# Kernel optimization log

Measured on AMD Instinct MI355X. Metric: run time of the kernel, lower is better.

The kernel has to match this reference:

```python
import jax, jax.numpy as jnp
import numpy as np

H, W = 512, 512
K = 10
N_ACTIONS = 8
HID1, HID2, HIDP = 32, 64, 32
# 8-neighborhood directions (i_dot, j_dot), as in env.DIRS
DIRS = [(-1, -1), (-1, 0), (-1, 1), (0, -1), (0, 1), (1, -1), (1, 0), (1, 1)]


def setup_inputs() -> dict:
    key = jax.random.key(0)
    ks = jax.random.split(key, 16)
    n_state = H * W
    w = lambda k, shape: (jax.random.normal(k, shape, dtype=jnp.float32) * 0.02)
    return {
        "x": jax.random.uniform(ks[0], (3, H, W), dtype=jnp.float32),
        "pos": jax.random.randint(ks[1], (2,), 0, H, dtype=jnp.int32),
        "W1": w(ks[2], (HID1, 3 * n_state)), "b1": jnp.zeros((HID1,), jnp.float32),
        "W2": w(ks[3], (HID2, HID1)), "b2": jnp.zeros((HID2,), jnp.float32),
        "Wro": w(ks[4], (n_state, HID2)), "bro": jnp.zeros((n_state,), jnp.float32),
        "Wri": w(ks[5], (n_state, HID2)), "bri": jnp.zeros((n_state,), jnp.float32),
        "Wp": w(ks[6], (n_state, HID2)), "bp": jnp.zeros((n_state,), jnp.float32),
        "Wpol": w(ks[7], (HIDP, 4 * n_state)), "bpol": jnp.zeros((HIDP,), jnp.float32),
        "Whead": w(ks[8], (N_ACTIONS, HIDP)), "bhead": jnp.zeros((N_ACTIONS,), jnp.float32),
    }


def reference(x, pos, W1, b1, W2, b2, Wro, bro, Wri, bri, Wp, bp, Wpol, bpol, Whead, bhead):
    state = x.reshape(-1)  # (3*H*W,)
    h = jax.nn.relu(W1 @ state + b1)
    h = jax.nn.relu(W2 @ h + b2)
    r_out = jax.nn.sigmoid(Wro @ h + bro).reshape(H, W)
    r_in = jax.nn.sigmoid(Wri @ h + bri).reshape(H, W)
    p = jax.nn.sigmoid(Wp @ h + bp).reshape(H, W)

    p_pad = jnp.pad(p, 1)
    rin_pad = jnp.pad(r_in, 1)
    rout_pad = jnp.pad(r_out, 1)

    def step(v, _):
        v_pad = jnp.pad(v, 1)  # (H+2, W+2)
        cands = []
        for i_dot, j_dot in DIRS:
            xs = j_dot + 1  # note: original code uses j_dot along axis 0
            ys = i_dot + 1
            cands.append(
                v_pad[xs:xs + H, ys:ys + W] * p_pad[xs:xs + H, ys:ys + W]
                + rin_pad[xs:xs + H, ys:ys + W] - rout_pad[xs:xs + H, ys:ys + W]
            )
        return jnp.max(jnp.stack(cands, 0), axis=0), None

    v, _ = jax.lax.scan(step, jnp.zeros((H, W), jnp.float32), None, length=K)

    inp_pol = jnp.concatenate([v.reshape(-1), state])  # (4*H*W,)
    logits = Whead @ jax.nn.relu(Wpol @ inp_pol + bpol) + bhead
    action_prob = jax.nn.softmax(logits, axis=-1)
    state_value = v[pos[0], pos[1]]
    return action_prob, state_value
```

## Files before the change

kernel.cpp:

```cpp
#include <hip/hip_runtime.h>

#define HW 512
#define NSTATE (HW * HW)
#define NC4_X 196608
#define NC4_POLROW 262144
#define NC4_V 65536

#define CH4 1024
#define NCH_X 192
#define SPAN_ROP 1024

#define WS_PART1 0
#define WS_PARTP 6144
#define WS_H2 14336
#define WS_P 14400
#define WS_RD (WS_P + NSTATE)
#define WS_V (WS_RD + NSTATE)

#define SGB __builtin_amdgcn_sched_group_barrier

__device__ __forceinline__ float wred(float a) {
  a += __shfl_xor(a, 32);
  a += __shfl_xor(a, 16);
  a += __shfl_xor(a, 8);
  a += __shfl_xor(a, 4);
  a += __shfl_xor(a, 2);
  a += __shfl_xor(a, 1);
  return a;
}

__device__ __forceinline__ float span_dot(const float4* __restrict__ wp,
                                          const float4* __restrict__ xp) {
  float acc = 0.f;
#pragma unroll
  for (int bt = 0; bt < 2; ++bt) {
    float4 w[8], xv[8];
#pragma unroll
    for (int j = 0; j < 8; ++j) w[j] = wp[bt * 512 + j * 64];
#pragma unroll
    for (int j = 0; j < 8; ++j) xv[j] = xp[bt * 512 + j * 64];
    SGB(0x020, 16, 0);
#pragma unroll
    for (int j = 0; j < 8; ++j)
      acc += w[j].x * xv[j].x + w[j].y * xv[j].y + w[j].z * xv[j].z +
             w[j].w * xv[j].w;
  }
  return acc;
}

__global__ __launch_bounds__(256) void mv_w1(const float4* __restrict__ W1,
                                             const float4* __restrict__ x,
                                             float* __restrict__ part1) {
  int b = blockIdx.x;
  int row = b / 48, cb = b - row * 48;
  int tid = threadIdx.x, wave = tid >> 6, lane = tid & 63;
  int ch = cb * 4 + wave;
  const float4* __restrict__ wp =
      W1 + (size_t)row * NC4_X + (size_t)ch * CH4 + lane;
  const float4* __restrict__ xp = x + (size_t)ch * CH4 + lane;
  float acc = span_dot(wp, xp);
  acc = wred(acc);
  if (lane == 0) part1[ch * 32 + row] = acc;
}

__global__ __launch_bounds__(1024) void finish_h(
    const float* __restrict__ partials, const float* __restrict__ b1,
    const float* __restrict__ W2, const float* __restrict__ b2,
    float* __restrict__ h2out) {
  __shared__ float red[32][32];
  __shared__ float h1[32];
  int tid = threadIdx.x;
  int row = tid & 31, grp = tid >> 5;
  float s = 0.f;
  for (int b = grp; b < NCH_X; b += 32) s += partials[b * 32 + row];
  red[grp][row] = s;
  __syncthreads();
  if (tid < 32) {
    float t = b1[tid];
    for (int g = 0; g < 32; ++g) t += red[g][tid];
    h1[tid] = fmaxf(t, 0.f);
  }
  __syncthreads();
  if (tid < 64) {
    float t = b2[tid];
    for (int k = 0; k < 32; ++k) t += W2[tid * 32 + k] * h1[k];
    h2out[tid] = fmaxf(t, 0.f);
  }
}

__global__ __launch_bounds__(256) void rop_kernel(
    const float4* __restrict__ Wro4, const float* __restrict__ bro,
    const float4* __restrict__ Wri4, const float* __restrict__ bri,
    const float4* __restrict__ Wp4, const float* __restrict__ bp,
    const float* __restrict__ h2, float* __restrict__ p_out,
    float* __restrict__ rd_out) {
  __shared__ float dots[4][3][64];
  int tid = threadIdx.x;
  int wave = tid >> 6, lane = tid & 63;
  int grp = lane >> 4;
  float4 h4 = ((const float4*)h2)[lane & 15];
  int span = blockIdx.x * 4 + wave;
  size_t base = (size_t)span * SPAN_ROP;
  const float4* mats[3] = {Wro4, Wri4, Wp4};
#pragma unroll
  for (int m = 0; m < 3; ++m) {
    const float4* __restrict__ W = mats[m] + base + lane;
#pragma unroll
    for (int batch = 0; batch < 2; ++batch) {
      float4 w[8];
#pragma unroll
      for (int j = 0; j < 8; ++j) w[j] = W[(batch * 8 + j) * 64];
      SGB(0x020, 8, 0);
      float part[8];
#pragma unroll
      for (int j = 0; j < 8; ++j)
        part[j] = w[j].x * h4.x + w[j].y * h4.y + w[j].z * h4.z + w[j].w * h4.w;
#pragma unroll
      for (int j = 0; j < 8; ++j) {
        part[j] += __shfl_xor(part[j], 8);
        part[j] += __shfl_xor(part[j], 4);
        part[j] += __shfl_xor(part[j], 2);
        part[j] += __shfl_xor(part[j], 1);
      }
      if ((lane & 15) == 0) {
#pragma unroll
        for (int j = 0; j < 8; ++j)
          dots[wave][m][(batch * 8 + j) * 4 + grp] = part[j];
      }
    }
  }
  __syncthreads();
  int o = blockIdx.x * 256 + tid;
  float dro = dots[tid >> 6][0][tid & 63] + bro[o];
  float dri = dots[tid >> 6][1][tid & 63] + bri[o];
  float dp = dots[tid >> 6][2][tid & 63] + bp[o];
  float sro = 1.f / (1.f + __expf(-dro));
  float sri = 1.f / (1.f + __expf(-dri));
  float pv = 1.f / (1.f + __expf(-dp));
  p_out[o] = pv;
  rd_out[o] = sri - sro;
}

#define VTILE 16
#define VHALO 10
#define ULW 44
#define ULH 38
__device__ __forceinline__ void row_win(const float* __restrict__ r,
                                        float e[6]) {
  float4 L = *reinterpret_cast<const float4*>(r - 4);
  float4 M = *reinterpret_cast<const float4*>(r);
  float4 R = *reinterpret_cast<const float4*>(r + 4);
  e[0] = L.w; e[1] = M.x; e[2] = M.y; e[3] = M.z; e[4] = M.w; e[5] = R.x;
}
__global__ __launch_bounds__(384) void valiter_kernel(
    const float* __restrict__ p, const float* __restrict__ rd,
    float* __restrict__ vout) {
  __shared__ float ua[ULH * ULW];
  __shared__ float ub[ULH * ULW];
  int tid = threadIdx.x;
  int blk = blockIdx.x;
  int ti = blk >> 5, tj = blk & 31;
  for (int idx = tid; idx < ULH * ULW; idx += 384) {
    ua[idx] = 0.f;
    ub[idx] = 0.f;
  }
  int i = tid / 9, j4 = tid - i * 9;
  bool active = (i < 36);
  int cb = 4 + 4 * j4;
  float pp[4], rr[4];
  if (active) {
    int gi = ti * VTILE - VHALO + i;
    int gj0 = tj * VTILE - VHALO + 4 * j4;
#pragma unroll
    for (int k = 0; k < 4; ++k) {
      int gj = gj0 + k;
      bool ok = (gi >= 0) & (gi < HW) & (gj >= 0) & (gj < HW);
      int gidx = gi * HW + gj;
      pp[k] = ok ? p[gidx] : 0.f;
      rr[k] = ok ? rd[gidx] : 0.f;
    }
  }
  __syncthreads();
  if (active) {
    *reinterpret_cast<float4*>(&ua[(i + 1) * ULW + cb]) =
        make_float4(rr[0], rr[1], rr[2], rr[3]);
  }
  __syncthreads();
  float* src = ua;
  float* dst = ub;
  for (int q = 0; q < 9; ++q) {
    int lo = q + 1, hi = 35 - q;
    if (active && i >= lo && i < hi && (4 * j4 + 4) > lo && (4 * j4) < hi) {
      float eA[6], eB[6], eC[6];
      row_win(src + i * ULW + cb, eA);
      row_win(src + (i + 1) * ULW + cb, eB);
      row_win(src + (i + 2) * ULW + cb, eC);
      float res[4];
#pragma unroll
      for (int k = 0; k < 4; ++k) {
        float a = fmaxf(fmaxf(eA[k], eA[k + 1]), eA[k + 2]);
        float c = fmaxf(fmaxf(eC[k], eC[k + 1]), eC[k + 2]);
        float b = fmaxf(eB[k], eB[k + 2]);
        float m = fmaxf(fmaxf(a, c), b);
        res[k] = m * pp[k] + rr[k];
      }
      *reinterpret_cast<float4*>(&dst[(i + 1) * ULW + cb]) =
          make_float4(res[0], res[1], res[2], res[3]);
    }
    __syncthreads();
    float* t_ = src;
    src = dst;
    dst = t_;
  }
  if (active && i >= 10 && i < 26 && (4 * j4 + 4) > 10 && (4 * j4) < 26) {
    float eA[6], eB[6], eC[6];
    row_win(src + i * ULW + cb, eA);
    row_win(src + (i + 1) * ULW + cb, eB);
    row_win(src + (i + 2) * ULW + cb, eC);
#pragma unroll
    for (int k = 0; k < 4; ++k) {
      int cj = 4 * j4 + k;
      if (cj >= 10 && cj < 26) {
        float a = fmaxf(fmaxf(eA[k], eA[k + 1]), eA[k + 2]);
        float c = fmaxf(fmaxf(eC[k], eC[k + 1]), eC[k + 2]);
        float b = fmaxf(eB[k], eB[k + 2]);
        float m = fmaxf(fmaxf(a, c), b);
        vout[(ti * VTILE + i - 10) * HW + tj * VTILE + cj - 10] = m;
      }
    }
  }
}

__global__ __launch_bounds__(256) void mv_pol(const float4* __restrict__ Wpol,
                                              const float4* __restrict__ x,
                                              const float4* __restrict__ v,
                                              float* __restrict__ partP) {
  int b = blockIdx.x;
  int tid = threadIdx.x, wave = tid >> 6, lane = tid & 63;
  int f = b * 4 + wave;
  int row = f >> 8, rc = f & 255;
  const float4* __restrict__ wp = Wpol + (size_t)f * CH4 + lane;
  const float4* __restrict__ xp =
      (rc < 64) ? (v + (size_t)rc * CH4 + lane)
                : (x + (size_t)(rc - 64) * CH4 + lane);
  float acc = span_dot(wp, xp);
  acc = wred(acc);
  if (lane == 0) partP[rc * 32 + row] = acc;
}

__global__ __launch_bounds__(1024) void finish_pol(
    const float* __restrict__ partP, const float* __restrict__ bpol,
    const float* __restrict__ Whead, const float* __restrict__ bhead,
    const float* __restrict__ v, const int* __restrict__ pos,
    float* __restrict__ out) {
  __shared__ float red[32][32];
  __shared__ float hp[32];
  __shared__ float logits[8];
  int tid = threadIdx.x;
  int row = tid & 31, grp = tid >> 5;
  float s = 0.f;
  for (int b = grp; b < 256; b += 32) s += partP[b * 32 + row];
  red[grp][row] = s;
  __syncthreads();
  if (tid < 32) {
    float t = bpol[tid];
    for (int g = 0; g < 32; ++g) t += red[g][tid];
    hp[tid] = fmaxf(t, 0.f);
  }
  __syncthreads();
  if (tid < 8) {
    float t = bhead[tid];
    for (int k = 0; k < 32; ++k) t += Whead[tid * 32 + k] * hp[k];
    logits[tid] = t;
  }
  __syncthreads();
  if (tid == 0) {
    float mx = logits[0];
    for (int j = 1; j < 8; ++j) mx = fmaxf(mx, logits[j]);
    float e[8], sum = 0.f;
    for (int j = 0; j < 8; ++j) {
      e[j] = __expf(logits[j] - mx);
      sum += e[j];
    }
    for (int j = 0; j < 8; ++j) out[j] = e[j] / sum;
    out[8] = v[pos[0] * HW + pos[1]];
  }
}

extern "C" void kernel_launch(void* const* d_in, const int* in_sizes, int n_in,
                              void* d_out, int out_size, void* d_ws,
                              size_t ws_size, hipStream_t stream) {
  const float* x = (const float*)d_in[0];
  const int* pos = (const int*)d_in[1];
  const float* W1 = (const float*)d_in[2];
  const float* b1 = (const float*)d_in[3];
  const float* W2 = (const float*)d_in[4];
  const float* b2 = (const float*)d_in[5];
  const float* Wro = (const float*)d_in[6];
  const float* bro = (const float*)d_in[7];
  const float* Wri = (const float*)d_in[8];
  const float* bri = (const float*)d_in[9];
  const float* Wp = (const float*)d_in[10];
  const float* bp = (const float*)d_in[11];
  const float* Wpol = (const float*)d_in[12];
  const float* bpol = (const float*)d_in[13];
  const float* Whead = (const float*)d_in[14];
  const float* bhead = (const float*)d_in[15];
  float* ws = (float*)d_ws;
  float* out = (float*)d_out;

  float* part1 = ws + WS_PART1;
  float* partP = ws + WS_PARTP;
  float* h2 = ws + WS_H2;
  float* pbuf = ws + WS_P;
  float* rdbuf = ws + WS_RD;
  float* vbuf = ws + WS_V;

  mv_w1<<<1536, 256, 0, stream>>>((const float4*)W1, (const float4*)x, part1);
  finish_h<<<1, 1024, 0, stream>>>(part1, b1, W2, b2, h2);
  rop_kernel<<<1024, 256, 0, stream>>>((const float4*)Wro, bro,
                                       (const float4*)Wri, bri,
                                       (const float4*)Wp, bp, h2, pbuf, rdbuf);
  valiter_kernel<<<1024, 384, 0, stream>>>(pbuf, rdbuf, vbuf);
  mv_pol<<<2048, 256, 0, stream>>>((const float4*)Wpol, (const float4*)x,
                                   (const float4*)vbuf, partP);
  finish_pol<<<1, 1024, 0, stream>>>(partP, bpol, Whead, bhead, vbuf, pos,
                                     out);
}
```

Baseline: 110.5 us.

## Split readout matvec per matrix and fuse sigmoid epilogue into value iteration

The readout kernel now gives each of the three weight matrices its own set of blocks, launching 3072 smaller blocks instead of 1024 blocks that each walk all three matrices. This is meant to raise memory-level parallelism on the weight stream. It writes raw dot products, and the bias add and sigmoids move into the value-iteration load stage. In exchange, value iteration reads three arrays plus three bias arrays instead of two, and recomputes sigmoids for halo cells that overlap between tiles.

```diff
diff --git a/kernel.cpp b/kernel.cpp
--- a/kernel.cpp
+++ b/kernel.cpp
@@ -8,14 +8,14 @@
 
 #define CH4 1024
 #define NCH_X 192
-#define SPAN_ROP 1024
 
 #define WS_PART1 0
 #define WS_PARTP 6144
 #define WS_H2 14336
-#define WS_P 14400
-#define WS_RD (WS_P + NSTATE)
-#define WS_V (WS_RD + NSTATE)
+#define WS_DRO 16384
+#define WS_DRI 278528
+#define WS_DP 540672
+#define WS_V 802816
 
 #define SGB __builtin_amdgcn_sched_group_barrier
 
@@ -88,57 +88,46 @@
   }
 }
 
-__global__ __launch_bounds__(256) void rop_kernel(
-    const float4* __restrict__ Wro4, const float* __restrict__ bro,
-    const float4* __restrict__ Wri4, const float* __restrict__ bri,
-    const float4* __restrict__ Wp4, const float* __restrict__ bp,
-    const float* __restrict__ h2, float* __restrict__ p_out,
-    float* __restrict__ rd_out) {
-  __shared__ float dots[4][3][64];
-  int tid = threadIdx.x;
-  int wave = tid >> 6, lane = tid & 63;
-  int grp = lane >> 4;
-  float4 h4 = ((const float4*)h2)[lane & 15];
-  int span = blockIdx.x * 4 + wave;
-  size_t base = (size_t)span * SPAN_ROP;
-  const float4* mats[3] = {Wro4, Wri4, Wp4};
-#pragma unroll
-  for (int m = 0; m < 3; ++m) {
-    const float4* __restrict__ W = mats[m] + base + lane;
-#pragma unroll
-    for (int batch = 0; batch < 2; ++batch) {
-      float4 w[8];
-#pragma unroll
-      for (int j = 0; j < 8; ++j) w[j] = W[(batch * 8 + j) * 64];
-      SGB(0x020, 8, 0);
-      float part[8];
-#pragma unroll
-      for (int j = 0; j < 8; ++j)
-        part[j] = w[j].x * h4.x + w[j].y * h4.y + w[j].z * h4.z + w[j].w * h4.w;
-#pragma unroll
-      for (int j = 0; j < 8; ++j) {
-        part[j] += __shfl_xor(part[j], 8);
-        part[j] += __shfl_xor(part[j], 4);
-        part[j] += __shfl_xor(part[j], 2);
-        part[j] += __shfl_xor(part[j], 1);
-      }
-      if ((lane & 15) == 0) {
-#pragma unroll
-        for (int j = 0; j < 8; ++j)
-          dots[wave][m][(batch * 8 + j) * 4 + grp] = part[j];
-      }
-    }
-  }
-  __syncthreads();
-  int o = blockIdx.x * 256 + tid;
-  float dro = dots[tid >> 6][0][tid & 63] + bro[o];
-  float dri = dots[tid >> 6][1][tid & 63] + bri[o];
-  float dp = dots[tid >> 6][2][tid & 63] + bp[o];
-  float sro = 1.f / (1.f + __expf(-dro));
-  float sri = 1.f / (1.f + __expf(-dri));
-  float pv = 1.f / (1.f + __expf(-dp));
-  p_out[o] = pv;
-  rd_out[o] = sri - sro;
+__global__ __launch_bounds__(256) void rop_part(
+    const float4* __restrict__ Wro4, const float4* __restrict__ Wri4,
+    const float4* __restrict__ Wp4, const float* __restrict__ h2,
+    float* __restrict__ dro, float* __restrict__ dri,
+    float* __restrict__ dp) {
+  __shared__ float dots[4][64];
+  int b = blockIdx.x;
+  int m = b >> 10;
+  int c = b & 1023;
+  int tid = threadIdx.x, wave = tid >> 6, lane = tid & 63;
+  int k = lane & 15, grp = lane >> 4;
+  const float4* __restrict__ W = (m == 0) ? Wro4 : ((m == 1) ? Wri4 : Wp4);
+  float* __restrict__ D = (m == 0) ? dro : ((m == 1) ? dri : dp);
+  float4 h4 = ((const float4*)h2)[k];
+  const float4* __restrict__ wp = W + ((size_t)c * 4 + wave) * 1024 + lane;
+  float part[16];
+#pragma unroll
+  for (int bt = 0; bt < 2; ++bt) {
+    float4 w[8];
+#pragma unroll
+    for (int j = 0; j < 8; ++j) w[j] = wp[(bt * 8 + j) * 64];
+    SGB(0x020, 8, 0);
+#pragma unroll
+    for (int j = 0; j < 8; ++j)
+      part[bt * 8 + j] =
+          w[j].x * h4.x + w[j].y * h4.y + w[j].z * h4.z + w[j].w * h4.w;
+  }
+#pragma unroll
+  for (int j = 0; j < 16; ++j) {
+    part[j] += __shfl_xor(part[j], 8);
+    part[j] += __shfl_xor(part[j], 4);
+    part[j] += __shfl_xor(part[j], 2);
+    part[j] += __shfl_xor(part[j], 1);
+  }
+  if (k == 0) {
+#pragma unroll
+    for (int j = 0; j < 16; ++j) dots[wave][j * 4 + grp] = part[j];
+  }
+  __syncthreads();
+  D[(size_t)c * 256 + tid] = dots[tid >> 6][tid & 63];
 }
 
 #define VTILE 16
@@ -153,7 +142,9 @@
   e[0] = L.w; e[1] = M.x; e[2] = M.y; e[3] = M.z; e[4] = M.w; e[5] = R.x;
 }
 __global__ __launch_bounds__(384) void valiter_kernel(
-    const float* __restrict__ p, const float* __restrict__ rd,
+    const float* __restrict__ dro, const float* __restrict__ dri,
+    const float* __restrict__ dp, const float* __restrict__ bro,
+    const float* __restrict__ bri, const float* __restrict__ bp,
     float* __restrict__ vout) {
   __shared__ float ua[ULH * ULW];
   __shared__ float ub[ULH * ULW];
@@ -175,9 +166,16 @@
     for (int k = 0; k < 4; ++k) {
       int gj = gj0 + k;
       bool ok = (gi >= 0) & (gi < HW) & (gj >= 0) & (gj < HW);
-      int gidx = gi * HW + gj;
-      pp[k] = ok ? p[gidx] : 0.f;
-      rr[k] = ok ? rd[gidx] : 0.f;
+      if (ok) {
+        int g = gi * HW + gj;
+        float sro = 1.f / (1.f + __expf(-(dro[g] + bro[g])));
+        float sri = 1.f / (1.f + __expf(-(dri[g] + bri[g])));
+        pp[k] = 1.f / (1.f + __expf(-(dp[g] + bp[g])));
+        rr[k] = sri - sro;
+      } else {
+        pp[k] = 0.f;
+        rr[k] = 0.f;
+      }
     }
   }
   __syncthreads();
@@ -312,16 +310,17 @@
   float* part1 = ws + WS_PART1;
   float* partP = ws + WS_PARTP;
   float* h2 = ws + WS_H2;
-  float* pbuf = ws + WS_P;
-  float* rdbuf = ws + WS_RD;
+  float* drob = ws + WS_DRO;
+  float* drib = ws + WS_DRI;
+  float* dpb = ws + WS_DP;
   float* vbuf = ws + WS_V;
 
   mv_w1<<<1536, 256, 0, stream>>>((const float4*)W1, (const float4*)x, part1);
   finish_h<<<1, 1024, 0, stream>>>(part1, b1, W2, b2, h2);
-  rop_kernel<<<1024, 256, 0, stream>>>((const float4*)Wro, bro,
-                                       (const float4*)Wri, bri,
-                                       (const float4*)Wp, bp, h2, pbuf, rdbuf);
-  valiter_kernel<<<1024, 384, 0, stream>>>(pbuf, rdbuf, vbuf);
+  rop_part<<<3072, 256, 0, stream>>>((const float4*)Wro, (const float4*)Wri,
+                                     (const float4*)Wp, h2, drob, drib, dpb);
+  valiter_kernel<<<1024, 384, 0, stream>>>(drob, drib, dpb, bro, bri, bp,
+                                           vbuf);
   mv_pol<<<2048, 256, 0, stream>>>((const float4*)Wpol, (const float4*)x,
                                    (const float4*)vbuf, partP);
   finish_pol<<<1, 1024, 0, stream>>>(partP, bpol, Whead, bhead, vbuf, pos,
```

New measurement: 115.3 us. 1.04x slower.
